# Performance work log

Measured on AMD Instinct MI355X. Metric: run time of the kernel, lower is better.

The kernel has to match this reference:

```python
import jax, jax.numpy as jnp
import numpy as np

B, M, C = 8, 1024, 768


def setup_inputs() -> dict:
    key = jax.random.key(0)
    ks = jax.random.split(key, 10)
    s = 0.02
    return {
        "layout_x": jax.random.normal(ks[0], (B, M, C), jnp.float32),
        "text_x": jax.random.normal(ks[1], (B, M, C), jnp.float32),
        "mask": jax.random.randint(ks[2], (B, M), 0, 2).astype(jnp.float32),
        "Wqkv": jax.random.normal(ks[3], (C, 3 * C), jnp.float32) * s,
        "bqkv": jnp.zeros((3 * C,), jnp.float32),
        "Wq": jax.random.normal(ks[4], (C, C), jnp.float32) * s,
        "bq": jnp.zeros((C,), jnp.float32),
        "Wkv": jax.random.normal(ks[5], (C, 2 * C), jnp.float32) * s,
        "bkv": jnp.zeros((2 * C,), jnp.float32),
        "Wffn": jax.random.normal(ks[6], (C, C), jnp.float32) * s,
        "bffn": jnp.zeros((C,), jnp.float32),
    }


def _masked_attn(q, k, v, pair_mask, scale):
    # pair_mask: [B,M,M] True where valid (mask_i * mask_j != 0)
    scores = jnp.einsum("bmd,bnd->bmn", q, k) * scale  # [B,M,M]
    scores = jnp.where(pair_mask, scores, jnp.float32(-10000.0))
    attn = jax.nn.softmax(scores, axis=-1)
    return jnp.einsum("bmn,bnd->bmd", attn, v)


def reference(layout_x, text_x, mask, Wqkv, bqkv, Wq, bq, Wkv, bkv, Wffn, bffn):
    dim = layout_x.shape[-1]
    scale = dim ** (-0.5)
    # mask repeated over C then mask@mask.T / C  ==  outer product of 1D masks
    pair = (mask[:, :, None] * mask[:, None, :]) != 0  # [B,M,M] bool, True=keep

    # self-attention on layout_x
    qkv = layout_x @ Wqkv + bqkv  # [B,M,3C]
    q, k, v = jnp.split(qkv, 3, axis=-1)
    layout_o = _masked_attn(q, k, v, pair, scale)

    # cross-attention: q from layout output, k/v from text_x
    cq = layout_o @ Wq + bq
    kv = text_x @ Wkv + bkv  # [B,M,2C]
    ck, cv = jnp.split(kv, 2, axis=-1)
    merge = _masked_attn(cq, ck, cv, pair, scale)

    return merge @ Wffn + bffn
```

## Files before the change

kernel.cpp:

```cpp
#include <hip/hip_runtime.h>
#include <math.h>

#define BDIM 8
#define MDIM 1024
#define CDIM 768
#define ROWS (BDIM * MDIM)

typedef __attribute__((ext_vector_type(8))) short short8;
typedef __attribute__((ext_vector_type(8))) unsigned short ushort8;
typedef __attribute__((ext_vector_type(4))) float f32x4;

#define MFMA16(a, b, c) __builtin_amdgcn_mfma_f32_16x16x32_bf16((a), (b), (c), 0, 0, 0)

#define BAR() __builtin_amdgcn_s_barrier()
#define FENCE() asm volatile("" ::: "memory")
#define SCHED_FENCE() __builtin_amdgcn_sched_barrier(0)
#define WAIT_LGKM0() asm volatile("s_waitcnt lgkmcnt(0)" ::: "memory")
#define WAIT_VM6() asm volatile("s_waitcnt vmcnt(6)" ::: "memory")
#define WAIT_VM0() asm volatile("s_waitcnt vmcnt(0)" ::: "memory")

__device__ __forceinline__ unsigned short f2bf(float f) {
  unsigned u = __float_as_uint(f);
  return (unsigned short)((u + 0x7FFFu + ((u >> 16) & 1u)) >> 16);
}

__global__ __launch_bounds__(256) void prologue(
    const float* __restrict__ xl, const float* __restrict__ xt,
    unsigned short* __restrict__ dxl, unsigned short* __restrict__ dxt,
    const float* __restrict__ W0, const float* __restrict__ W1,
    const float* __restrict__ W2, const float* __restrict__ W3,
    unsigned short* __restrict__ D0, unsigned short* __restrict__ D1,
    unsigned short* __restrict__ D2, unsigned short* __restrict__ D3) {
  const int bx = blockIdx.x;
  const int tid = threadIdx.x;
  if (bx < 6144) {
    const float* src = bx < 3072 ? xl : xt;
    unsigned short* dst = bx < 3072 ? dxl : dxt;
    const int i = ((bx < 3072 ? bx : bx - 3072) * 256 + tid) * 8;
    const float4 a = *(const float4*)(src + i);
    const float4 b = *(const float4*)(src + i + 4);
    ushort8 o;
    o[0] = f2bf(a.x); o[1] = f2bf(a.y); o[2] = f2bf(a.z); o[3] = f2bf(a.w);
    o[4] = f2bf(b.x); o[5] = f2bf(b.y); o[6] = f2bf(b.z); o[7] = f2bf(b.w);
    *(ushort8*)(dst + i) = o;
  } else {
    int x = bx - 6144;
    int bxx = x % 168;
    const int k0 = (x / 168) * 32;
    const float* W; unsigned short* D; int N;
    if (bxx < 72)       { W = W0; D = D0; N = 2304; }
    else if (bxx < 96)  { W = W1; D = D1; N = 768;  bxx -= 72; }
    else if (bxx < 144) { W = W2; D = D2; N = 1536; bxx -= 96; }
    else                { W = W3; D = D3; N = 768;  bxx -= 144; }
    __shared__ unsigned short t[32][33];
    const int tx = tid & 31, ty = tid >> 5;
    const int n0 = bxx * 32;
#pragma unroll
    for (int i = 0; i < 4; ++i)
      t[ty + i * 8][tx] = f2bf(W[(size_t)(k0 + ty + i * 8) * N + n0 + tx]);
    __syncthreads();
#pragma unroll
    for (int i = 0; i < 4; ++i)
      D[(size_t)(n0 + ty + i * 8) * CDIM + k0 + tx] = t[tx][ty + i * 8];
  }
}

template <int J>
__device__ __forceinline__ void stageJ(
    const unsigned short* __restrict__ g, int ld, int k0,
    unsigned short* lds, int wave, int lane) {
  const int gchunk = (lane & 7) ^ (lane >> 3);
#pragma unroll
  for (int j = 0; j < J; ++j) {
    const int grp = wave * J + j;
    const unsigned short* gp =
        g + (size_t)(grp * 8 + (lane >> 3)) * ld + k0 + gchunk * 8;
    __builtin_amdgcn_global_load_lds(
        (const __attribute__((address_space(1))) unsigned int*)gp,
        (__attribute__((address_space(3))) unsigned int*)(lds + grp * 512),
        16, 0, 0);
  }
}

__device__ __forceinline__ void mfma_loop64h(
    const unsigned short* __restrict__ A, int lda,
    const unsigned short* __restrict__ Bt, int ldb, int K,
    unsigned short* As, unsigned short* Bs, f32x4 acc[2][4],
    int wave, int lane) {
  const int wx = wave & 1, wy = wave >> 1;
  const int quad = lane >> 4, l16 = lane & 15;
  for (int k0 = 0; k0 < K; k0 += 64) {
    stageJ<2>(A, lda, k0, As, wave, lane);
    stageJ<4>(Bt, ldb, k0, Bs, wave, lane);
    __syncthreads();
#pragma unroll
    for (int h = 0; h < 2; ++h) {
      const int slot = ((((h << 2) | quad) ^ (l16 & 7))) * 8;
      short8 afr[2], bfr[4];
#pragma unroll
      for (int mt = 0; mt < 2; ++mt)
        afr[mt] = *(const short8*)&As[(wy * 32 + mt * 16 + l16) * 64 + slot];
#pragma unroll
      for (int nt = 0; nt < 4; ++nt)
        bfr[nt] = *(const short8*)&Bs[(wx * 64 + nt * 16 + l16) * 64 + slot];
#pragma unroll
      for (int mt = 0; mt < 2; ++mt)
#pragma unroll
        for (int nt = 0; nt < 4; ++nt)
          acc[mt][nt] = MFMA16(afr[mt], bfr[nt], acc[mt][nt]);
    }
    __syncthreads();
  }
}

__device__ __forceinline__ void read_fragsA(
    const unsigned short* h, int roff, short8 fr[4][2], int l16, int quad) {
#pragma unroll
  for (int mf = 0; mf < 4; ++mf)
#pragma unroll
    for (int kh = 0; kh < 2; ++kh) {
      const int slot = (((kh << 2) | quad) ^ (l16 & 7)) * 8;
      fr[mf][kh] = *(const short8*)&h[(roff + mf * 16 + l16) * 64 + slot];
    }
}

__device__ __forceinline__ void read_fragsB(
    const unsigned short* h, int roff, short8 fr[2][2], int l16, int quad) {
#pragma unroll
  for (int nf = 0; nf < 2; ++nf)
#pragma unroll
    for (int kh = 0; kh < 2; ++kh) {
      const int slot = (((kh << 2) | quad) ^ (l16 & 7)) * 8;
      fr[nf][kh] = *(const short8*)&h[(roff + nf * 16 + l16) * 64 + slot];
    }
}

#define MFMA_PHASE(GM, GN, BB)                                              \
  do {                                                                      \
    SCHED_FENCE();                                                          \
    __builtin_amdgcn_s_setprio(1);                                          \
    _Pragma("unroll") for (int mf = 0; mf < 4; ++mf)                        \
    _Pragma("unroll") for (int nf = 0; nf < 2; ++nf)                        \
    _Pragma("unroll") for (int kh = 0; kh < 2; ++kh)                        \
        acc[GM][GN][mf][nf] =                                               \
            MFMA16(afr[mf][kh], BB[nf][kh], acc[GM][GN][mf][nf]);           \
    __builtin_amdgcn_s_setprio(0);                                          \
    SCHED_FENCE();                                                          \
  } while (0)

__global__ __launch_bounds__(512, 2) void gemm_qkvkv(
    const unsigned short* __restrict__ A0g, const unsigned short* __restrict__ B0g,
    const float* __restrict__ bias0, unsigned short* __restrict__ Y0,
    unsigned short* __restrict__ vT0,
    const unsigned short* __restrict__ A1g, const unsigned short* __restrict__ B1g,
    const float* __restrict__ bias1, unsigned short* __restrict__ Y1,
    unsigned short* __restrict__ vT1) {
  __shared__ __align__(16) unsigned short lds[65536];
  int lin = blockIdx.x;
  const unsigned short *A, *Bt; const float* bias;
  unsigned short *Y, *vTd; int lastSlice, m0, c0;
  if (lin < 288) {
    A = A0g; Bt = B0g; bias = bias0; Y = Y0; vTd = vT0; lastSlice = 2;
    const int xcd = lin & 7, j = lin >> 3;
    m0 = (xcd * 4 + (j & 3)) * 256; c0 = (j >> 2) * 256;
  } else {
    lin -= 288;
    A = A1g; Bt = B1g; bias = bias1; Y = Y1; vTd = vT1; lastSlice = 1;
    const int xcd = lin & 7, j = lin >> 3;
    m0 = (xcd * 4 + (j & 3)) * 256; c0 = (j >> 2) * 256;
  }
  const int tid = threadIdx.x;
  const int wave = tid >> 6, lane = tid & 63;
  const int wy = wave >> 2, wx = wave & 3;
  const int quad = lane >> 4, l16 = lane & 15;

  const unsigned short* Ah[2] = {A + (size_t)m0 * CDIM,
                                 A + (size_t)(m0 + 128) * CDIM};
  const unsigned short* Bh[2] = {Bt + (size_t)c0 * CDIM,
                                 Bt + (size_t)(c0 + 128) * CDIM};

  const f32x4 vzero = {0.f, 0.f, 0.f, 0.f};
  f32x4 acc[2][2][4][2];
#pragma unroll
  for (int gm = 0; gm < 2; ++gm)
#pragma unroll
    for (int gn = 0; gn < 2; ++gn)
#pragma unroll
      for (int mf = 0; mf < 4; ++mf)
#pragma unroll
        for (int nf = 0; nf < 2; ++nf) acc[gm][gn][mf][nf] = vzero;
  short8 afr[4][2], b0r[2][2], b1r[2][2];

  stageJ<2>(Ah[0], CDIM, 0, lds + 0, wave, lane);
  stageJ<2>(Bh[0], CDIM, 0, lds + 16384, wave, lane);
  stageJ<2>(Bh[1], CDIM, 0, lds + 24576, wave, lane);
  stageJ<2>(Ah[1], CDIM, 0, lds + 8192, wave, lane);
  stageJ<2>(Ah[0], CDIM, 64, lds + 32768 + 0, wave, lane);
  stageJ<2>(Bh[0], CDIM, 64, lds + 32768 + 16384, wave, lane);
  stageJ<2>(Bh[1], CDIM, 64, lds + 32768 + 24576, wave, lane);
  WAIT_VM6();
  BAR(); FENCE();

  for (int t = 0; t < 12; ++t) {
    unsigned short* bufc = lds + (t & 1) * 32768;
    unsigned short* bufn = lds + ((t + 1) & 1) * 32768;
    read_fragsA(bufc + 0, wy * 64, afr, l16, quad);
    read_fragsB(bufc + 16384, wx * 32, b0r, l16, quad);
    if (t < 11) stageJ<2>(Ah[1], CDIM, (t + 1) * 64, bufn + 8192, wave, lane);
    BAR(); WAIT_LGKM0();
    MFMA_PHASE(0, 0, b0r);
    read_fragsB(bufc + 24576, wx * 32, b1r, l16, quad);
    BAR(); WAIT_LGKM0();
    MFMA_PHASE(0, 1, b1r);
    read_fragsA(bufc + 8192, wy * 64, afr, l16, quad);
    if (t < 10) stageJ<2>(Ah[0], CDIM, (t + 2) * 64, bufc + 0, wave, lane);
    BAR(); WAIT_LGKM0();
    MFMA_PHASE(1, 0, b0r);
    if (t < 10) {
      stageJ<2>(Bh[0], CDIM, (t + 2) * 64, bufc + 16384, wave, lane);
      stageJ<2>(Bh[1], CDIM, (t + 2) * 64, bufc + 24576, wave, lane);
      WAIT_VM6();
    } else if (t == 10) {
      WAIT_VM0();
    }
    BAR(); FENCE();
    MFMA_PHASE(1, 1, b1r);
  }

#pragma unroll
  for (int gm = 0; gm < 2; ++gm)
#pragma unroll
    for (int gn = 0; gn < 2; ++gn) {
      const int cb2 = c0 + gn * 128 + wx * 32;
      const int slice = cb2 / 768;
      const int rb = m0 + gm * 128 + wy * 64;
      if (slice == lastSlice) {
#pragma unroll
        for (int mf = 0; mf < 4; ++mf) {
          const int row0 = rb + mf * 16 + quad * 4;
          const int b = row0 >> 10, n0 = row0 & 1023;
#pragma unroll
          for (int nf = 0; nf < 2; ++nf) {
            const int gcol = cb2 + nf * 16 + l16;
            const int d = gcol - slice * 768;
            const float bv = bias[gcol];
            uint2 o;
            o.x = (unsigned)f2bf(acc[gm][gn][mf][nf][0] + bv) |
                  ((unsigned)f2bf(acc[gm][gn][mf][nf][1] + bv) << 16);
            o.y = (unsigned)f2bf(acc[gm][gn][mf][nf][2] + bv) |
                  ((unsigned)f2bf(acc[gm][gn][mf][nf][3] + bv) << 16);
            *(uint2*)&vTd[((size_t)b * CDIM + d) * MDIM + n0] = o;
          }
        }
      } else {
        const size_t sbase = (size_t)slice * ROWS * 768;
#pragma unroll
        for (int mf = 0; mf < 4; ++mf)
#pragma unroll
          for (int nf = 0; nf < 2; ++nf) {
            const int gcol = cb2 + nf * 16 + l16;
            const int lcol = gcol - slice * 768;
            const float bv = bias[gcol];
#pragma unroll
            for (int rg = 0; rg < 4; ++rg) {
              const int row = rb + mf * 16 + quad * 4 + rg;
              Y[sbase + (size_t)row * 768 + lcol] =
                  f2bf(acc[gm][gn][mf][nf][rg] + bv);
            }
          }
      }
    }
}

__global__ __launch_bounds__(256, 4) void gemm_proj64(
    const unsigned short* __restrict__ A, const unsigned short* __restrict__ Bt,
    const float* __restrict__ bias, unsigned short* __restrict__ Y) {
  __shared__ __align__(16) unsigned short As[64 * 64];
  __shared__ __align__(16) unsigned short Bs[128 * 64];
  const int lin = blockIdx.x;
  const int xcd = lin & 7, j = lin >> 3;
  const int m0 = (xcd * 16 + (j & 15)) * 64;
  const int c0 = (j >> 4) * 128;
  const int tid = threadIdx.x;
  const int wave = tid >> 6, lane = tid & 63;
  const int wx = wave & 1, wy = wave >> 1;
  const int quad = lane >> 4, l16 = lane & 15;
  const f32x4 vzero = {0.f, 0.f, 0.f, 0.f};
  f32x4 acc[2][4];
#pragma unroll
  for (int mt = 0; mt < 2; ++mt)
#pragma unroll
    for (int nt = 0; nt < 4; ++nt) acc[mt][nt] = vzero;
  mfma_loop64h(A + (size_t)m0 * CDIM, CDIM, Bt + (size_t)c0 * CDIM, CDIM,
               CDIM, As, Bs, acc, wave, lane);
#pragma unroll
  for (int mt = 0; mt < 2; ++mt)
#pragma unroll
    for (int nt = 0; nt < 4; ++nt) {
      const int col = c0 + wx * 64 + nt * 16 + l16;
      const float bv = bias[col];
#pragma unroll
      for (int rg = 0; rg < 4; ++rg) {
        const int row = m0 + wy * 32 + mt * 16 + quad * 4 + rg;
        Y[(size_t)row * 768 + col] = f2bf(acc[mt][nt][rg] + bv);
      }
    }
}

__global__ __launch_bounds__(256, 4) void gemm_ffn64(
    const unsigned short* __restrict__ A, const unsigned short* __restrict__ Bt,
    const float* __restrict__ bias, float* __restrict__ Y) {
  __shared__ __align__(16) unsigned short As[64 * 64];
  __shared__ __align__(16) unsigned short Bs[128 * 64];
  const int lin = blockIdx.x;
  const int xcd = lin & 7, j = lin >> 3;
  const int m0 = (xcd * 16 + (j & 15)) * 64;
  const int c0 = (j >> 4) * 128;
  const int tid = threadIdx.x;
  const int wave = tid >> 6, lane = tid & 63;
  const int wx = wave & 1, wy = wave >> 1;
  const int quad = lane >> 4, l16 = lane & 15;
  const f32x4 vzero = {0.f, 0.f, 0.f, 0.f};
  f32x4 acc[2][4];
#pragma unroll
  for (int mt = 0; mt < 2; ++mt)
#pragma unroll
    for (int nt = 0; nt < 4; ++nt) acc[mt][nt] = vzero;
  mfma_loop64h(A + (size_t)m0 * CDIM, CDIM, Bt + (size_t)c0 * CDIM, CDIM,
               CDIM, As, Bs, acc, wave, lane);
#pragma unroll
  for (int mt = 0; mt < 2; ++mt)
#pragma unroll
    for (int nt = 0; nt < 4; ++nt) {
      const int col = c0 + wx * 64 + nt * 16 + l16;
      const float bv = bias[col];
#pragma unroll
      for (int rg = 0; rg < 4; ++rg) {
        const int row = m0 + wy * 32 + mt * 16 + quad * 4 + rg;
        Y[(size_t)row * 768 + col] = acc[mt][nt][rg] + bv;
      }
    }
}

__global__ __launch_bounds__(256, 4) void gemm_qk64(
    const unsigned short* __restrict__ Qb, const unsigned short* __restrict__ Kb,
    const float* __restrict__ mask, unsigned short* __restrict__ S, float scale,
    float* __restrict__ rsp) {
  __shared__ __align__(16) unsigned short As[64 * 64];
  __shared__ __align__(16) unsigned short Bs[128 * 64];
  const int c0 = blockIdx.x * 128;
  const int m0 = blockIdx.y * 64;
  const int b = blockIdx.z;
  const int tid = threadIdx.x;
  const int wave = tid >> 6, lane = tid & 63;
  const int wx = wave & 1, wy = wave >> 1;
  const int quad = lane >> 4, l16 = lane & 15;

  const f32x4 vzero = {0.f, 0.f, 0.f, 0.f};
  f32x4 acc[2][4];
#pragma unroll
  for (int mt = 0; mt < 2; ++mt)
#pragma unroll
    for (int nt = 0; nt < 4; ++nt) acc[mt][nt] = vzero;

  mfma_loop64h(Qb + ((size_t)b * MDIM + m0) * CDIM, CDIM,
               Kb + ((size_t)b * MDIM + c0) * CDIM, CDIM, CDIM,
               As, Bs, acc, wave, lane);

  const float* maskb = mask + b * MDIM;
  float mrow[2][4], rsum[2][4];
#pragma unroll
  for (int mt = 0; mt < 2; ++mt)
#pragma unroll
    for (int rg = 0; rg < 4; ++rg) {
      mrow[mt][rg] = maskb[m0 + wy * 32 + mt * 16 + quad * 4 + rg];
      rsum[mt][rg] = 0.f;
    }
  unsigned short* Sb = S + (size_t)b * MDIM * MDIM;
#pragma unroll
  for (int nt = 0; nt < 4; ++nt) {
    const int col = c0 + wx * 64 + nt * 16 + l16;
    const float mcol = maskb[col];
#pragma unroll
    for (int mt = 0; mt < 2; ++mt)
#pragma unroll
      for (int rg = 0; rg < 4; ++rg) {
        const int row = m0 + wy * 32 + mt * 16 + quad * 4 + rg;
        const float e = (mrow[mt][rg] * mcol != 0.f)
                            ? __expf(acc[mt][nt][rg] * scale)
                            : 1e-30f;
        Sb[(size_t)row * MDIM + col] = f2bf(e);
        rsum[mt][rg] += e;
      }
  }
  for (int off = 1; off < 16; off <<= 1) {
#pragma unroll
    for (int mt = 0; mt < 2; ++mt)
#pragma unroll
      for (int rg = 0; rg < 4; ++rg)
        rsum[mt][rg] += __shfl_xor(rsum[mt][rg], off, 64);
  }
  if (l16 == 0) {
    float* rs = rsp + ((((size_t)blockIdx.x * 2 + wx) * 8 + b) << 10) +
                m0 + wy * 32;
#pragma unroll
    for (int mt = 0; mt < 2; ++mt)
#pragma unroll
      for (int rg = 0; rg < 4; ++rg)
        rs[mt * 16 + quad * 4 + rg] = rsum[mt][rg];
  }
}

__global__ __launch_bounds__(256, 4) void attn_pv64(
    const unsigned short* __restrict__ P, const unsigned short* __restrict__ vT,
    unsigned short* __restrict__ O, const float* __restrict__ rsp) {
  __shared__ __align__(16) unsigned short As[64 * 64];
  __shared__ __align__(16) unsigned short Bs[128 * 64];
  const int c0 = blockIdx.x * 128;
  const int m0 = blockIdx.y * 64;
  const int b = blockIdx.z;
  const int tid = threadIdx.x;
  const int wave = tid >> 6, lane = tid & 63;
  const int wx = wave & 1, wy = wave >> 1;
  const int quad = lane >> 4, l16 = lane & 15;

  const f32x4 vzero = {0.f, 0.f, 0.f, 0.f};
  f32x4 acc[2][4];
#pragma unroll
  for (int mt = 0; mt < 2; ++mt)
#pragma unroll
    for (int nt = 0; nt < 4; ++nt) acc[mt][nt] = vzero;

  mfma_loop64h(P + ((size_t)b * MDIM + m0) * MDIM, MDIM,
               vT + ((size_t)b * CDIM + c0) * MDIM, MDIM, MDIM,
               As, Bs, acc, wave, lane);

  const float* rsb = rsp + (((size_t)l16 * 8 + b) << 10) + m0 + wy * 32;
  float inv[2][4];
#pragma unroll
  for (int mt = 0; mt < 2; ++mt)
#pragma unroll
    for (int rg = 0; rg < 4; ++rg) {
      float s = rsb[mt * 16 + quad * 4 + rg];
      for (int off = 1; off < 16; off <<= 1) s += __shfl_xor(s, off, 64);
      inv[mt][rg] = 1.f / s;
    }
#pragma unroll
  for (int mt = 0; mt < 2; ++mt)
#pragma unroll
    for (int nt = 0; nt < 4; ++nt)
#pragma unroll
      for (int rg = 0; rg < 4; ++rg) {
        const int row = m0 + wy * 32 + mt * 16 + quad * 4 + rg;
        const int col = c0 + wx * 64 + nt * 16 + l16;
        O[(size_t)(b * MDIM + row) * CDIM + col] =
            f2bf(acc[mt][nt][rg] * inv[mt][rg]);
      }
}

extern "C" void kernel_launch(void* const* d_in, const int* in_sizes, int n_in,
                              void* d_out, int out_size, void* d_ws, size_t ws_size,
                              hipStream_t stream) {
  const float* layout_x = (const float*)d_in[0];
  const float* text_x   = (const float*)d_in[1];
  const float* maskp    = (const float*)d_in[2];
  const float* Wqkv     = (const float*)d_in[3];
  const float* bqkv     = (const float*)d_in[4];
  const float* Wq       = (const float*)d_in[5];
  const float* bq       = (const float*)d_in[6];
  const float* Wkv      = (const float*)d_in[7];
  const float* bkv      = (const float*)d_in[8];
  const float* Wffn     = (const float*)d_in[9];
  const float* bffn     = (const float*)d_in[10];
  float* out = (float*)d_out;
  char* ws = (char*)d_ws;

  const float scale = 1.0f / sqrtf((float)CDIM);

  unsigned short* xlb    = (unsigned short*)(ws);
  unsigned short* xtb    = (unsigned short*)(ws + 12582912);
  unsigned short* Wqkv_t = (unsigned short*)(ws + 25165824);
  unsigned short* Wq_t   = (unsigned short*)(ws + 28704768);
  unsigned short* Wkv_t  = (unsigned short*)(ws + 29884416);
  unsigned short* Wffn_t = (unsigned short*)(ws + 32243712);
  unsigned short* Qb     = (unsigned short*)(ws + 33423360);
  unsigned short* Kb     = (unsigned short*)(ws + 46006272);
  unsigned short* vT     = (unsigned short*)(ws + 58589184);
  unsigned short* S      = (unsigned short*)(ws + 71172096);
  unsigned short* attn1  = xlb;
  unsigned short* cqb    = Qb;
  unsigned short* cK  = (unsigned short*)out;
  unsigned short* cVT = (unsigned short*)out + 6291456;
  float* rsp = (float*)xtb;

  prologue<<<10176, 256, 0, stream>>>(layout_x, text_x, xlb, xtb,
                                      Wqkv, Wq, Wkv, Wffn,
                                      Wqkv_t, Wq_t, Wkv_t, Wffn_t);
  gemm_qkvkv<<<480, 512, 0, stream>>>(xlb, Wqkv_t, bqkv, Qb, vT,
                                      xtb, Wkv_t, bkv, cK, cVT);
  gemm_qk64<<<dim3(8, 16, BDIM), 256, 0, stream>>>(Qb, Kb, maskp, S, scale, rsp);
  attn_pv64<<<dim3(6, 16, BDIM), 256, 0, stream>>>(S, vT, attn1, rsp);
  gemm_proj64<<<768, 256, 0, stream>>>(attn1, Wq_t, bq, cqb);
  gemm_qk64<<<dim3(8, 16, BDIM), 256, 0, stream>>>(cqb, cK, maskp, S, scale, rsp);
  attn_pv64<<<dim3(6, 16, BDIM), 256, 0, stream>>>(S, cVT, attn1, rsp);
  gemm_ffn64<<<768, 256, 0, stream>>>(attn1, Wffn_t, bffn, out);
}
```

Measured before the change: 312.2 us.

## Software-pipeline LDS fragment reads across MFMA phases in QKV GEMM

Restructures the main K-loop of the QKV/KV projection GEMM so that LDS fragment reads for the next MFMA phase are issued before the current phase, using double A-fragment registers and partial lgkmcnt/vmcnt waits instead of full drains. Global staging is split into one stage per phase, and the last two iterations are peeled with explicit wait counts. Raw ds_read_b128 inline asm with precomputed byte offsets replaces the pointer-based helpers. This is meant to hide LDS latency behind MFMA work, at the cost of more registers and fragile hand-tuned wait counts that could race.

```diff
diff --git a/kernel.cpp b/kernel.cpp
--- a/kernel.cpp
+++ b/kernel.cpp
@@ -16,12 +16,23 @@
 #define FENCE() asm volatile("" ::: "memory")
 #define SCHED_FENCE() __builtin_amdgcn_sched_barrier(0)
 #define WAIT_LGKM0() asm volatile("s_waitcnt lgkmcnt(0)" ::: "memory")
+#define WAIT_LGKM4() asm volatile("s_waitcnt lgkmcnt(4)" ::: "memory")
+#define WAIT_LGKM8() asm volatile("s_waitcnt lgkmcnt(8)" ::: "memory")
+#define WAIT_VM8() asm volatile("s_waitcnt vmcnt(8)" ::: "memory")
 #define WAIT_VM6() asm volatile("s_waitcnt vmcnt(6)" ::: "memory")
+#define WAIT_VM4() asm volatile("s_waitcnt vmcnt(4)" ::: "memory")
+#define WAIT_VM2() asm volatile("s_waitcnt vmcnt(2)" ::: "memory")
 #define WAIT_VM0() asm volatile("s_waitcnt vmcnt(0)" ::: "memory")
 
 __device__ __forceinline__ unsigned short f2bf(float f) {
   unsigned u = __float_as_uint(f);
   return (unsigned short)((u + 0x7FFFu + ((u >> 16) & 1u)) >> 16);
+}
+
+__device__ __forceinline__ short8 dsr128(unsigned off) {
+  short8 r;
+  asm volatile("ds_read_b128 %0, %1" : "=v"(r) : "v"(off));
+  return r;
 }
 
 __global__ __launch_bounds__(256) void prologue(
@@ -113,29 +124,7 @@
   }
 }
 
-__device__ __forceinline__ void read_fragsA(
-    const unsigned short* h, int roff, short8 fr[4][2], int l16, int quad) {
-#pragma unroll
-  for (int mf = 0; mf < 4; ++mf)
-#pragma unroll
-    for (int kh = 0; kh < 2; ++kh) {
-      const int slot = (((kh << 2) | quad) ^ (l16 & 7)) * 8;
-      fr[mf][kh] = *(const short8*)&h[(roff + mf * 16 + l16) * 64 + slot];
-    }
-}
-
-__device__ __forceinline__ void read_fragsB(
-    const unsigned short* h, int roff, short8 fr[2][2], int l16, int quad) {
-#pragma unroll
-  for (int nf = 0; nf < 2; ++nf)
-#pragma unroll
-    for (int kh = 0; kh < 2; ++kh) {
-      const int slot = (((kh << 2) | quad) ^ (l16 & 7)) * 8;
-      fr[nf][kh] = *(const short8*)&h[(roff + nf * 16 + l16) * 64 + slot];
-    }
-}
-
-#define MFMA_PHASE(GM, GN, BB)                                              \
+#define MFMA_PHASE(GM, GN, AA, BB)                                          \
   do {                                                                      \
     SCHED_FENCE();                                                          \
     __builtin_amdgcn_s_setprio(1);                                          \
@@ -143,9 +132,24 @@
     _Pragma("unroll") for (int nf = 0; nf < 2; ++nf)                        \
     _Pragma("unroll") for (int kh = 0; kh < 2; ++kh)                        \
         acc[GM][GN][mf][nf] =                                               \
-            MFMA16(afr[mf][kh], BB[nf][kh], acc[GM][GN][mf][nf]);           \
+            MFMA16(AA[mf][kh], BB[nf][kh], acc[GM][GN][mf][nf]);            \
     __builtin_amdgcn_s_setprio(0);                                          \
     SCHED_FENCE();                                                          \
+  } while (0)
+
+#define RD_A(dst, base)                                                     \
+  do {                                                                      \
+    _Pragma("unroll") for (int mf = 0; mf < 4; ++mf) {                      \
+      dst[mf][0] = dsr128((base) + aRow[mf] + sl0);                         \
+      dst[mf][1] = dsr128((base) + aRow[mf] + sl1);                         \
+    }                                                                       \
+  } while (0)
+#define RD_B(dst, base)                                                     \
+  do {                                                                      \
+    _Pragma("unroll") for (int nf = 0; nf < 2; ++nf) {                      \
+      dst[nf][0] = dsr128((base) + bRow[nf] + sl0);                         \
+      dst[nf][1] = dsr128((base) + bRow[nf] + sl1);                         \
+    }                                                                       \
   } while (0)
 
 __global__ __launch_bounds__(512, 2) void gemm_qkvkv(
@@ -179,6 +183,16 @@
   const unsigned short* Bh[2] = {Bt + (size_t)c0 * CDIM,
                                  Bt + (size_t)(c0 + 128) * CDIM};
 
+  const unsigned sl0 = (unsigned)((quad ^ (l16 & 7)) * 16);
+  const unsigned sl1 = (unsigned)(((4 | quad) ^ (l16 & 7)) * 16);
+  unsigned aRow[4], bRow[2];
+#pragma unroll
+  for (int mf = 0; mf < 4; ++mf)
+    aRow[mf] = (unsigned)((wy * 64 + mf * 16 + l16) * 128);
+#pragma unroll
+  for (int nf = 0; nf < 2; ++nf)
+    bRow[nf] = (unsigned)((wx * 32 + nf * 16 + l16) * 128);
+
   const f32x4 vzero = {0.f, 0.f, 0.f, 0.f};
   f32x4 acc[2][2][4][2];
 #pragma unroll
@@ -189,7 +203,7 @@
       for (int mf = 0; mf < 4; ++mf)
 #pragma unroll
         for (int nf = 0; nf < 2; ++nf) acc[gm][gn][mf][nf] = vzero;
-  short8 afr[4][2], b0r[2][2], b1r[2][2];
+  short8 afrE[4][2], afrO[4][2], b0r[2][2], b1r[2][2];
 
   stageJ<2>(Ah[0], CDIM, 0, lds + 0, wave, lane);
   stageJ<2>(Bh[0], CDIM, 0, lds + 16384, wave, lane);
@@ -198,33 +212,66 @@
   stageJ<2>(Ah[0], CDIM, 64, lds + 32768 + 0, wave, lane);
   stageJ<2>(Bh[0], CDIM, 64, lds + 32768 + 16384, wave, lane);
   stageJ<2>(Bh[1], CDIM, 64, lds + 32768 + 24576, wave, lane);
-  WAIT_VM6();
+  WAIT_VM8();
   BAR(); FENCE();
-
-  for (int t = 0; t < 12; ++t) {
-    unsigned short* bufc = lds + (t & 1) * 32768;
-    unsigned short* bufn = lds + ((t + 1) & 1) * 32768;
-    read_fragsA(bufc + 0, wy * 64, afr, l16, quad);
-    read_fragsB(bufc + 16384, wx * 32, b0r, l16, quad);
-    if (t < 11) stageJ<2>(Ah[1], CDIM, (t + 1) * 64, bufn + 8192, wave, lane);
-    BAR(); WAIT_LGKM0();
-    MFMA_PHASE(0, 0, b0r);
-    read_fragsB(bufc + 24576, wx * 32, b1r, l16, quad);
-    BAR(); WAIT_LGKM0();
-    MFMA_PHASE(0, 1, b1r);
-    read_fragsA(bufc + 8192, wy * 64, afr, l16, quad);
-    if (t < 10) stageJ<2>(Ah[0], CDIM, (t + 2) * 64, bufc + 0, wave, lane);
-    BAR(); WAIT_LGKM0();
-    MFMA_PHASE(1, 0, b0r);
-    if (t < 10) {
-      stageJ<2>(Bh[0], CDIM, (t + 2) * 64, bufc + 16384, wave, lane);
-      stageJ<2>(Bh[1], CDIM, (t + 2) * 64, bufc + 24576, wave, lane);
-      WAIT_VM6();
-    } else if (t == 10) {
-      WAIT_VM0();
-    }
-    BAR(); FENCE();
-    MFMA_PHASE(1, 1, b1r);
+  RD_A(afrE, 0u);
+  RD_B(b0r, 32768u);
+
+  for (int t = 0; t < 10; ++t) {
+    unsigned short* bufcP = lds + (t & 1) * 32768;
+    unsigned short* bufnP = lds + ((t + 1) & 1) * 32768;
+    const unsigned bc = (unsigned)((t & 1) * 65536);
+    const unsigned bn = (unsigned)(((t + 1) & 1) * 65536);
+    RD_B(b1r, bc + 49152u);
+    stageJ<2>(Ah[1], CDIM, (t + 1) * 64, bufnP + 8192, wave, lane);
+    WAIT_VM8(); BAR(); WAIT_LGKM4();
+    MFMA_PHASE(0, 0, afrE, b0r);
+    RD_A(afrO, bc + 16384u);
+    stageJ<2>(Ah[0], CDIM, (t + 2) * 64, bufcP + 0, wave, lane);
+    WAIT_VM8(); BAR(); WAIT_LGKM8();
+    MFMA_PHASE(0, 1, afrE, b1r);
+    RD_A(afrE, bn + 0u);
+    stageJ<2>(Bh[0], CDIM, (t + 2) * 64, bufcP + 16384, wave, lane);
+    WAIT_VM8(); BAR(); WAIT_LGKM8();
+    MFMA_PHASE(1, 0, afrO, b0r);
+    RD_B(b0r, bn + 32768u);
+    stageJ<2>(Bh[1], CDIM, (t + 2) * 64, bufcP + 24576, wave, lane);
+    WAIT_VM8(); BAR();
+    MFMA_PHASE(1, 1, afrO, b1r);
+  }
+  {
+    const unsigned bc = 0u, bn = 65536u;
+    unsigned short* bufnP = lds + 32768;
+    RD_B(b1r, bc + 49152u);
+    stageJ<2>(Ah[1], CDIM, 11 * 64, bufnP + 8192, wave, lane);
+    WAIT_VM8(); BAR(); WAIT_LGKM4();
+    MFMA_PHASE(0, 0, afrE, b0r);
+
+    RD_A(afrO, bc + 16384u);
+    WAIT_VM6(); BAR(); WAIT_LGKM8();
+    MFMA_PHASE(0, 1, afrE, b1r);
+
+    RD_A(afrE, bn + 0u);
+    WAIT_VM4(); BAR(); WAIT_LGKM8();
+    MFMA_PHASE(1, 0, afrO, b0r);
+
+    RD_B(b0r, bn + 32768u);
+    WAIT_VM2(); BAR();
+    MFMA_PHASE(1, 1, afrO, b1r);
+  }
+  {
+    const unsigned bc = 65536u;
+    RD_B(b1r, bc + 49152u);
+    WAIT_VM0(); BAR(); WAIT_LGKM4();
+    MFMA_PHASE(0, 0, afrE, b0r);
+
+    RD_A(afrO, bc + 16384u);
+    WAIT_LGKM8();
+    MFMA_PHASE(0, 1, afrE, b1r);
+
+    WAIT_LGKM0();
+    MFMA_PHASE(1, 0, afrO, b0r);
+    MFMA_PHASE(1, 1, afrO, b1r);
   }
 
 #pragma unroll
```

Result: no change. 306.1 us (-1.9%).
